# Kernel optimization log

Hardware: AMD Instinct MI355X
Metric: run time of the kernel (lower is better)

Reference implementation:

```python
import jax, jax.numpy as jnp
import numpy as np

N_NODES = 100000
N_EDGES = 1600000
IN_FEATS = 128
H_FEATS = 128


def setup_inputs() -> dict:
    key = jax.random.key(0)
    ks = jax.random.split(key, 8)
    s_in = 1.0 / np.sqrt(IN_FEATS)
    s_h = 1.0 / np.sqrt(H_FEATS)
    return {
        "emb_weight": jax.random.normal(ks[0], (N_NODES, IN_FEATS), jnp.float32),
        "W1_self": jax.random.normal(ks[1], (IN_FEATS, H_FEATS), jnp.float32) * s_in,
        "W1_neigh": jax.random.normal(ks[2], (IN_FEATS, H_FEATS), jnp.float32) * s_in,
        "b1": jnp.zeros((H_FEATS,), jnp.float32),
        "W2_self": jax.random.normal(ks[3], (H_FEATS, H_FEATS), jnp.float32) * s_h,
        "W2_neigh": jax.random.normal(ks[4], (H_FEATS, H_FEATS), jnp.float32) * s_h,
        "b2": jnp.zeros((H_FEATS,), jnp.float32),
        "edges": jax.random.randint(ks[5], (2, N_EDGES), 0, N_NODES, jnp.int64)
            if jax.config.jax_enable_x64 else
            jax.random.randint(ks[5], (2, N_EDGES), 0, N_NODES, jnp.int32),
    }


def _sage_conv(h, src, dst, W_self, W_neigh, b):
    # DGL SAGEConv(mean): out = h @ W_self + mean_neigh(h) @ W_neigh + b
    agg = jax.ops.segment_sum(h[src], dst, num_segments=N_NODES)  # [N, F]
    deg = jax.ops.segment_sum(jnp.ones((src.shape[0],), h.dtype), dst,
                              num_segments=N_NODES)
    mean = agg / jnp.maximum(deg, 1.0)[:, None]  # zero-in-degree -> zeros
    return h @ W_self + mean @ W_neigh + b


def reference(emb_weight, W1_self, W1_neigh, b1, W2_self, W2_neigh, b2, edges):
    src, dst = edges[0], edges[1]
    h = emb_weight  # node_emb(g.nodes()) over all nodes
    h = _sage_conv(h, src, dst, W1_self, W1_neigh, b1)
    h = jax.nn.leaky_relu(h, negative_slope=0.2)
    # dropout is identity in eval mode
    h = _sage_conv(h, src, dst, W2_self, W2_neigh, b2)
    return h
```

## Files before the change

kernel.cpp:

```cpp
#include <hip/hip_runtime.h>
#include <hip/hip_bf16.h>

#define N_NODES_C 100000
#define FEATS 128
#define SH 10
#define NBK 128
#define PB  256
#define CAST_BLOCKS 12500

typedef unsigned int uint32;
typedef __bf16 bf16_t;
typedef bf16_t bf16x8 __attribute__((ext_vector_type(8)));
typedef float f32x4 __attribute__((ext_vector_type(4)));

union Frag { uint4 u; bf16x8 v; };

__device__ __forceinline__ unsigned short f32_to_bf16_bits(float f) {
    uint32 u = __float_as_uint(f);
    u += 0x7fffu + ((u >> 16) & 1u);
    return (unsigned short)(u >> 16);
}
__device__ __forceinline__ float bf16_lo(uint32 p) { return __uint_as_float(p << 16); }
__device__ __forceinline__ float bf16_hi(uint32 p) { return __uint_as_float(p & 0xffff0000u); }

__global__ __launch_bounds__(256) void prep_fused(
    const int* __restrict__ dst, int* __restrict__ gHist, int nE, int chunk,
    const float4* __restrict__ emb4, unsigned short* __restrict__ hb0, int n4,
    const float* __restrict__ W1s, const float* __restrict__ W1n, unsigned short* __restrict__ wt1,
    const float* __restrict__ W2s, const float* __restrict__ W2n, unsigned short* __restrict__ wt2)
{
    __shared__ int h[NBK];
    const int b = blockIdx.x;
    const int tid = threadIdx.x;

    if (b < PB) {
        if (tid < NBK) h[tid] = 0;
        __syncthreads();
        const int b0 = b * chunk;
        const int e1 = min(b0 + chunk, nE);
        for (int e = b0 + tid; e < e1; e += 256)
            atomicAdd(&h[dst[e] >> SH], 1);
        __syncthreads();
        if (tid < NBK) gHist[tid * PB + b] = h[tid];
    } else if (b < PB + 32) {
        const int which = (b - PB) >> 4;
        const float* Ws = which ? W2s : W1s;
        const float* Wn = which ? W2n : W1n;
        unsigned short* wt = which ? wt2 : wt1;
        int gid = ((b - PB) & 15) * 256 + tid;
        int frag = gid >> 6, lane = gid & 63;
        int nt = frag >> 3, ks = frag & 7;
        int n = nt * 16 + (lane & 15);
        int kbase = ks * 32 + (lane >> 4) * 8;
        union { unsigned short s[8]; uint4 u; } o;
#pragma unroll
        for (int j = 0; j < 8; ++j) {
            int k = kbase + j;
            float v = (k < 128) ? Ws[(size_t)k * FEATS + n] : Wn[(size_t)(k - 128) * FEATS + n];
            o.s[j] = f32_to_bf16_bits(v);
        }
        *(uint4*)(wt + (size_t)gid * 8) = o.u;
    } else {
        int i = (b - PB - 32) * 256 + tid;
        if (i >= n4) return;
        float4 v = emb4[i];
        union { unsigned short s[4]; uint2 u; } o;
        o.s[0] = f32_to_bf16_bits(v.x);
        o.s[1] = f32_to_bf16_bits(v.y);
        o.s[2] = f32_to_bf16_bits(v.z);
        o.s[3] = f32_to_bf16_bits(v.w);
        *(uint2*)(hb0 + (size_t)i * 4) = o.u;
    }
}

__global__ __launch_bounds__(1024) void scan_one(int* __restrict__ g) {
    __shared__ int ss[1024];
    const int tid = threadIdx.x;
    const int base = tid * 32;
    int pref[32];
    int sum = 0;
#pragma unroll
    for (int j = 0; j < 32; ++j) {
        int v = g[base + j];
        pref[j] = sum;
        sum += v;
    }
    ss[tid] = sum;
    __syncthreads();
    for (int d = 1; d < 1024; d <<= 1) {
        int t = (tid >= d) ? ss[tid - d] : 0;
        __syncthreads();
        ss[tid] += t;
        __syncthreads();
    }
    int ex = ss[tid] - sum;
#pragma unroll
    for (int j = 0; j < 32; ++j)
        g[base + j] = ex + pref[j];
}

__global__ __launch_bounds__(1024) void part_scatter(const int* __restrict__ src,
                                                     const int* __restrict__ dst,
                                                     const int* __restrict__ gScan,
                                                     uint32* __restrict__ ebuf,
                                                     int nE, int chunk) {
    __shared__ int cur[NBK];
    const int tid = threadIdx.x;
    if (tid < NBK) cur[tid] = gScan[tid * PB + blockIdx.x];
    __syncthreads();
    const int b0 = blockIdx.x * chunk;
    const int e1 = min(b0 + chunk, nE);
    for (int e = b0 + tid; e < e1; e += 1024) {
        int d = dst[e];
        int pos = atomicAdd(&cur[d >> SH], 1);
        ebuf[pos] = (uint32)src[e] | ((uint32)(d & ((1 << SH) - 1)) << 17);
    }
}

__global__ __launch_bounds__(1024) void bucket_csr(const uint32* __restrict__ ebuf,
                                                   const int* __restrict__ gScan,
                                                   int* __restrict__ off,
                                                   int* __restrict__ csr,
                                                   int nE) {
    __shared__ int cnt[1 << SH];
    __shared__ int ss[1 << SH];
    const int b = blockIdx.x;
    const int tid = threadIdx.x;
    const int start = gScan[b * PB];
    const int end = gScan[(b + 1) * PB];
    const int nodeBase = b << SH;
    cnt[tid] = 0;
    __syncthreads();
    for (int e = start + tid; e < end; e += 1024)
        atomicAdd(&cnt[ebuf[e] >> 17], 1);
    __syncthreads();
    int own = cnt[tid];
    ss[tid] = own;
    __syncthreads();
    for (int d = 1; d < 1024; d <<= 1) {
        int t = (tid >= d) ? ss[tid - d] : 0;
        __syncthreads();
        ss[tid] += t;
        __syncthreads();
    }
    int ex = ss[tid] - own;
    cnt[tid] = ex;
    int node = nodeBase + tid;
    if (node < N_NODES_C) off[node] = start + ex;
    if (b == gridDim.x - 1 && tid == 0) off[N_NODES_C] = nE;
    __syncthreads();
    for (int e = start + tid; e < end; e += 1024) {
        uint32 p = ebuf[e];
        int pos = atomicAdd(&cnt[p >> 17], 1);
        csr[start + pos] = (int)((p & 0x1FFFFu) << 8);
    }
}

__global__ __launch_bounds__(256) void gather_mean_w2(const unsigned short* __restrict__ hb,
                                                      const int* __restrict__ csrB,
                                                      const int* __restrict__ off,
                                                      unsigned short* __restrict__ meanb,
                                                      int nNodes) {
    const int node = blockIdx.x * 4 + (threadIdx.x >> 6);
    const int lane = threadIdx.x & 63;
    if (node >= nNodes) return;
    const int start = __builtin_amdgcn_readfirstlane(off[node]);
    const int end   = __builtin_amdgcn_readfirstlane(off[node + 1]);
    const int half = lane >> 5;
    const int c = lane & 31;
    const char* base = (const char*)hb + (size_t)(c * 8);
    float a0 = 0.f, a1 = 0.f, a2 = 0.f, a3 = 0.f;
    int e = start;
    for (; e + 16 <= end; e += 16) {
        const int o0  = csrB[e + 0],  o1  = csrB[e + 1],  o2  = csrB[e + 2],  o3  = csrB[e + 3];
        const int o4  = csrB[e + 4],  o5  = csrB[e + 5],  o6  = csrB[e + 6],  o7  = csrB[e + 7];
        const int o8  = csrB[e + 8],  o9  = csrB[e + 9],  o10 = csrB[e + 10], o11 = csrB[e + 11];
        const int o12 = csrB[e + 12], o13 = csrB[e + 13], o14 = csrB[e + 14], o15 = csrB[e + 15];
        const uint2 u0 = *(const uint2*)(base + (size_t)(half ? o1  : o0));
        const uint2 u1 = *(const uint2*)(base + (size_t)(half ? o3  : o2));
        const uint2 u2 = *(const uint2*)(base + (size_t)(half ? o5  : o4));
        const uint2 u3 = *(const uint2*)(base + (size_t)(half ? o7  : o6));
        const uint2 u4 = *(const uint2*)(base + (size_t)(half ? o9  : o8));
        const uint2 u5 = *(const uint2*)(base + (size_t)(half ? o11 : o10));
        const uint2 u6 = *(const uint2*)(base + (size_t)(half ? o13 : o12));
        const uint2 u7 = *(const uint2*)(base + (size_t)(half ? o15 : o14));
        a0 += bf16_lo(u0.x); a1 += bf16_hi(u0.x); a2 += bf16_lo(u0.y); a3 += bf16_hi(u0.y);
        a0 += bf16_lo(u1.x); a1 += bf16_hi(u1.x); a2 += bf16_lo(u1.y); a3 += bf16_hi(u1.y);
        a0 += bf16_lo(u2.x); a1 += bf16_hi(u2.x); a2 += bf16_lo(u2.y); a3 += bf16_hi(u2.y);
        a0 += bf16_lo(u3.x); a1 += bf16_hi(u3.x); a2 += bf16_lo(u3.y); a3 += bf16_hi(u3.y);
        a0 += bf16_lo(u4.x); a1 += bf16_hi(u4.x); a2 += bf16_lo(u4.y); a3 += bf16_hi(u4.y);
        a0 += bf16_lo(u5.x); a1 += bf16_hi(u5.x); a2 += bf16_lo(u5.y); a3 += bf16_hi(u5.y);
        a0 += bf16_lo(u6.x); a1 += bf16_hi(u6.x); a2 += bf16_lo(u6.y); a3 += bf16_hi(u6.y);
        a0 += bf16_lo(u7.x); a1 += bf16_hi(u7.x); a2 += bf16_lo(u7.y); a3 += bf16_hi(u7.y);
    }
    if (e + 8 <= end) {
        const int o0 = csrB[e + 0], o1 = csrB[e + 1], o2 = csrB[e + 2], o3 = csrB[e + 3];
        const int o4 = csrB[e + 4], o5 = csrB[e + 5], o6 = csrB[e + 6], o7 = csrB[e + 7];
        const uint2 u0 = *(const uint2*)(base + (size_t)(half ? o1 : o0));
        const uint2 u1 = *(const uint2*)(base + (size_t)(half ? o3 : o2));
        const uint2 u2 = *(const uint2*)(base + (size_t)(half ? o5 : o4));
        const uint2 u3 = *(const uint2*)(base + (size_t)(half ? o7 : o6));
        a0 += bf16_lo(u0.x); a1 += bf16_hi(u0.x); a2 += bf16_lo(u0.y); a3 += bf16_hi(u0.y);
        a0 += bf16_lo(u1.x); a1 += bf16_hi(u1.x); a2 += bf16_lo(u1.y); a3 += bf16_hi(u1.y);
        a0 += bf16_lo(u2.x); a1 += bf16_hi(u2.x); a2 += bf16_lo(u2.y); a3 += bf16_hi(u2.y);
        a0 += bf16_lo(u3.x); a1 += bf16_hi(u3.x); a2 += bf16_lo(u3.y); a3 += bf16_hi(u3.y);
        e += 8;
    }
    if (e + 4 <= end) {
        const int o0 = csrB[e + 0], o1 = csrB[e + 1], o2 = csrB[e + 2], o3 = csrB[e + 3];
        const uint2 u0 = *(const uint2*)(base + (size_t)(half ? o1 : o0));
        const uint2 u1 = *(const uint2*)(base + (size_t)(half ? o3 : o2));
        a0 += bf16_lo(u0.x); a1 += bf16_hi(u0.x); a2 += bf16_lo(u0.y); a3 += bf16_hi(u0.y);
        a0 += bf16_lo(u1.x); a1 += bf16_hi(u1.x); a2 += bf16_lo(u1.y); a3 += bf16_hi(u1.y);
        e += 4;
    }
    if (e + 2 <= end) {
        const int o0 = csrB[e + 0], o1 = csrB[e + 1];
        const uint2 u = *(const uint2*)(base + (size_t)(half ? o1 : o0));
        a0 += bf16_lo(u.x); a1 += bf16_hi(u.x); a2 += bf16_lo(u.y); a3 += bf16_hi(u.y);
        e += 2;
    }
    if (e < end && half == 0) {
        const uint2 u = *(const uint2*)(base + (size_t)csrB[e]);
        a0 += bf16_lo(u.x); a1 += bf16_hi(u.x); a2 += bf16_lo(u.y); a3 += bf16_hi(u.y);
    }
    a0 += __shfl_xor(a0, 32);
    a1 += __shfl_xor(a1, 32);
    a2 += __shfl_xor(a2, 32);
    a3 += __shfl_xor(a3, 32);
    const int deg = end - start;
    const float invd = (deg > 0) ? (1.f / (float)deg) : 0.f;
    if (half == 0) {
        uint2 o;
        o.x = ((uint32)f32_to_bf16_bits(a1 * invd) << 16) | (uint32)f32_to_bf16_bits(a0 * invd);
        o.y = ((uint32)f32_to_bf16_bits(a3 * invd) << 16) | (uint32)f32_to_bf16_bits(a2 * invd);
        ((uint2*)meanb)[(size_t)node * 32 + c] = o;
    }
}

__global__ __launch_bounds__(512) void sage_gemm_mfma(const unsigned short* __restrict__ HB,
                                                      const unsigned short* __restrict__ MB,
                                                      const unsigned short* __restrict__ WT,
                                                      const float* __restrict__ bias,
                                                      void* __restrict__ OUTP,
                                                      int nNodes, int mode) {
    __shared__ uint4 wtl[4096];
    const int tid = threadIdx.x;
    const uint4* wt4 = (const uint4*)WT;
#pragma unroll
    for (int i = 0; i < 8; ++i)
        wtl[i * 512 + tid] = wt4[i * 512 + tid];

    const int wave = tid >> 6;
    const int lane = tid & 63;
    const int waveBase = blockIdx.x * 128 + wave * 16;
    const int m = lane & 15;
    const int quad = lane >> 4;

    int arow = waveBase + m;
    if (arow >= nNodes) arow = nNodes - 1;
    const uint4* hrow = (const uint4*)(HB + (size_t)arow * FEATS);
    const uint4* mrow = (const uint4*)(MB + (size_t)arow * FEATS);

    Frag a[8];
#pragma unroll
    for (int ks = 0; ks < 4; ++ks) a[ks].u = hrow[ks * 4 + quad];
#pragma unroll
    for (int ks = 0; ks < 4; ++ks) a[ks + 4].u = mrow[ks * 4 + quad];

    __syncthreads();

    f32x4 acc[8];
#pragma unroll
    for (int nt = 0; nt < 8; ++nt) acc[nt] = (f32x4){0.f, 0.f, 0.f, 0.f};

#pragma unroll
    for (int ks = 0; ks < 8; ++ks) {
#pragma unroll
        for (int nt = 0; nt < 8; ++nt) {
            Frag b;
            b.u = wtl[(nt * 8 + ks) * 64 + lane];
            acc[nt] = __builtin_amdgcn_mfma_f32_16x16x32_bf16(a[ks].v, b.v, acc[nt], 0, 0, 0);
        }
    }

#pragma unroll
    for (int nt = 0; nt < 8; ++nt) {
        const int col = nt * 16 + m;
        const float bv = bias[col];
#pragma unroll
        for (int r = 0; r < 4; ++r) {
            const int grow = waveBase + quad * 4 + r;
            if (grow >= nNodes) continue;
            float v = acc[nt][r] + bv;
            if (mode) {
                v = v > 0.f ? v : 0.2f * v;
                ((unsigned short*)OUTP)[(size_t)grow * FEATS + col] = f32_to_bf16_bits(v);
            } else {
                ((float*)OUTP)[(size_t)grow * FEATS + col] = v;
            }
        }
    }
}

extern "C" void kernel_launch(void* const* d_in, const int* in_sizes, int n_in,
                              void* d_out, int out_size, void* d_ws, size_t ws_size,
                              hipStream_t stream) {
    const float* emb = (const float*)d_in[0];
    const float* W1s = (const float*)d_in[1];
    const float* W1n = (const float*)d_in[2];
    const float* b1  = (const float*)d_in[3];
    const float* W2s = (const float*)d_in[4];
    const float* W2n = (const float*)d_in[5];
    const float* b2  = (const float*)d_in[6];
    const int*   edg = (const int*)d_in[7];

    const int nE = in_sizes[7] / 2;
    const int* src = edg;
    const int* dst = edg + nE;

    const int chunk = (nE + PB - 1) / PB;
    const int nActB = (N_NODES_C + (1 << SH) - 1) >> SH;
    const int n4 = N_NODES_C * FEATS / 4;

    const size_t bfTab = (size_t)N_NODES_C * FEATS * sizeof(unsigned short);

    char* ws = (char*)d_ws;
    int* off      = (int*)(ws);
    int* gHist    = (int*)(ws + (512 << 10));
    int* csr      = (int*)(ws + (1 << 20));
    uint32* ebuf  = (uint32*)(ws + (8 << 20));
    unsigned short* wt1 = (unsigned short*)(ws + (15 << 20));
    unsigned short* wt2 = (unsigned short*)(ws + (15 << 20) + (64 << 10));
    unsigned short* hb0 = (unsigned short*)(ws + (16 << 20));
    unsigned short* h1b = (unsigned short*)((char*)hb0 + bfTab);
    unsigned short* mnb = (unsigned short*)((char*)h1b + bfTab);
    float* out = (float*)d_out;

    prep_fused<<<PB + 32 + CAST_BLOCKS, 256, 0, stream>>>(
        dst, gHist, nE, chunk, (const float4*)emb, hb0, n4,
        W1s, W1n, wt1, W2s, W2n, wt2);

    scan_one<<<1, 1024, 0, stream>>>(gHist);
    part_scatter<<<PB, 1024, 0, stream>>>(src, dst, gHist, ebuf, nE, chunk);
    bucket_csr<<<nActB, 1024, 0, stream>>>(ebuf, gHist, off, csr, nE);

    const int gatherBlocks = (N_NODES_C + 3) / 4;
    const int gemmBlocks = (N_NODES_C + 127) / 128;

    gather_mean_w2<<<gatherBlocks, 256, 0, stream>>>(hb0, csr, off, mnb, N_NODES_C);
    sage_gemm_mfma<<<gemmBlocks, 512, 0, stream>>>(hb0, mnb, wt1, b1, h1b, N_NODES_C, 1);

    gather_mean_w2<<<gatherBlocks, 256, 0, stream>>>(h1b, csr, off, mnb, N_NODES_C);
    sage_gemm_mfma<<<gemmBlocks, 512, 0, stream>>>(h1b, mnb, wt2, b2, out, N_NODES_C, 0);
}
```

Before: 321.4 us.

## Fold global scan into scatter blocks and make GEMM persistent over row stripes

Removes the single-block scan kernel: every part_scatter block now redundantly scans the 32K-entry histogram and keeps only its own bucket cursors, and block 0 writes the bucket start offsets for bucket_csr. The GEMM becomes a grid-stride persistent kernel with 512 blocks, so each block loads the weight tile into LDS once and reuses it across several 128-row stripes. This saves a launch and a serial single-block step, and cuts the number of weight tile loads. In exchange each scatter block repeats the scan, and the GEMM no longer overlaps one stripe's A loads with another block's work as naturally.

```diff
diff --git a/kernel.cpp b/kernel.cpp
--- a/kernel.cpp
+++ b/kernel.cpp
@@ -73,40 +73,48 @@
     }
 }
 
-__global__ __launch_bounds__(1024) void scan_one(int* __restrict__ g) {
+__global__ __launch_bounds__(1024) void part_scatter(const int* __restrict__ src,
+                                                     const int* __restrict__ dst,
+                                                     const int* __restrict__ gHist,
+                                                     int* __restrict__ bstart,
+                                                     uint32* __restrict__ ebuf,
+                                                     int nE, int chunk) {
     __shared__ int ss[1024];
+    __shared__ int cur[NBK];
     const int tid = threadIdx.x;
     const int base = tid * 32;
     int pref[32];
-    int sum = 0;
-#pragma unroll
-    for (int j = 0; j < 32; ++j) {
-        int v = g[base + j];
-        pref[j] = sum;
-        sum += v;
-    }
-    ss[tid] = sum;
-    __syncthreads();
-    for (int d = 1; d < 1024; d <<= 1) {
-        int t = (tid >= d) ? ss[tid - d] : 0;
-        __syncthreads();
-        ss[tid] += t;
-        __syncthreads();
-    }
-    int ex = ss[tid] - sum;
-#pragma unroll
-    for (int j = 0; j < 32; ++j)
-        g[base + j] = ex + pref[j];
-}
-
-__global__ __launch_bounds__(1024) void part_scatter(const int* __restrict__ src,
-                                                     const int* __restrict__ dst,
-                                                     const int* __restrict__ gScan,
-                                                     uint32* __restrict__ ebuf,
-                                                     int nE, int chunk) {
-    __shared__ int cur[NBK];
-    const int tid = threadIdx.x;
-    if (tid < NBK) cur[tid] = gScan[tid * PB + blockIdx.x];
+    {
+        int sum = 0;
+#pragma unroll
+        for (int j = 0; j < 32; ++j) {
+            int v = gHist[base + j];
+            pref[j] = sum;
+            sum += v;
+        }
+        ss[tid] = sum;
+        __syncthreads();
+        for (int d = 1; d < 1024; d <<= 1) {
+            int t = (tid >= d) ? ss[tid - d] : 0;
+            __syncthreads();
+            ss[tid] += t;
+            __syncthreads();
+        }
+        const int ex = ss[tid] - sum;
+#pragma unroll
+        for (int j = 0; j < 32; ++j) {
+            const int f = base + j;
+            const int v = ex + pref[j];
+            if ((f & (PB - 1)) == blockIdx.x) cur[f >> 8] = v;
+        }
+        if (blockIdx.x == 0) {
+#pragma unroll
+            for (int j = 0; j < 32; ++j) {
+                const int f = base + j;
+                if ((f & (PB - 1)) == 0) bstart[f >> 8] = ex + pref[j];
+            }
+        }
+    }
     __syncthreads();
     const int b0 = blockIdx.x * chunk;
     const int e1 = min(b0 + chunk, nE);
@@ -118,7 +126,7 @@
 }
 
 __global__ __launch_bounds__(1024) void bucket_csr(const uint32* __restrict__ ebuf,
-                                                   const int* __restrict__ gScan,
+                                                   const int* __restrict__ bstart,
                                                    int* __restrict__ off,
                                                    int* __restrict__ csr,
                                                    int nE) {
@@ -126,8 +134,8 @@
     __shared__ int ss[1 << SH];
     const int b = blockIdx.x;
     const int tid = threadIdx.x;
-    const int start = gScan[b * PB];
-    const int end = gScan[(b + 1) * PB];
+    const int start = bstart[b];
+    const int end = bstart[b + 1];
     const int nodeBase = b << SH;
     cnt[tid] = 0;
     __syncthreads();
@@ -243,7 +251,7 @@
                                                       const unsigned short* __restrict__ WT,
                                                       const float* __restrict__ bias,
                                                       void* __restrict__ OUTP,
-                                                      int nNodes, int mode) {
+                                                      int nNodes, int nStripes, int mode) {
     __shared__ uint4 wtl[4096];
     const int tid = threadIdx.x;
     const uint4* wt4 = (const uint4*)WT;
@@ -253,51 +261,54 @@
 
     const int wave = tid >> 6;
     const int lane = tid & 63;
-    const int waveBase = blockIdx.x * 128 + wave * 16;
     const int m = lane & 15;
     const int quad = lane >> 4;
 
-    int arow = waveBase + m;
-    if (arow >= nNodes) arow = nNodes - 1;
-    const uint4* hrow = (const uint4*)(HB + (size_t)arow * FEATS);
-    const uint4* mrow = (const uint4*)(MB + (size_t)arow * FEATS);
-
-    Frag a[8];
-#pragma unroll
-    for (int ks = 0; ks < 4; ++ks) a[ks].u = hrow[ks * 4 + quad];
-#pragma unroll
-    for (int ks = 0; ks < 4; ++ks) a[ks + 4].u = mrow[ks * 4 + quad];
-
-    __syncthreads();
-
-    f32x4 acc[8];
-#pragma unroll
-    for (int nt = 0; nt < 8; ++nt) acc[nt] = (f32x4){0.f, 0.f, 0.f, 0.f};
-
-#pragma unroll
-    for (int ks = 0; ks < 8; ++ks) {
+    __syncthreads();
+
+    for (int stripe = blockIdx.x; stripe < nStripes; stripe += gridDim.x) {
+        const int waveBase = stripe * 128 + wave * 16;
+
+        int arow = waveBase + m;
+        if (arow >= nNodes) arow = nNodes - 1;
+        const uint4* hrow = (const uint4*)(HB + (size_t)arow * FEATS);
+        const uint4* mrow = (const uint4*)(MB + (size_t)arow * FEATS);
+
+        Frag a[8];
+#pragma unroll
+        for (int ks = 0; ks < 4; ++ks) a[ks].u = hrow[ks * 4 + quad];
+#pragma unroll
+        for (int ks = 0; ks < 4; ++ks) a[ks + 4].u = mrow[ks * 4 + quad];
+
+        f32x4 acc[8];
+#pragma unroll
+        for (int nt = 0; nt < 8; ++nt) acc[nt] = (f32x4){0.f, 0.f, 0.f, 0.f};
+
+#pragma unroll
+        for (int ks = 0; ks < 8; ++ks) {
+#pragma unroll
+            for (int nt = 0; nt < 8; ++nt) {
+                Frag b;
+                b.u = wtl[(nt * 8 + ks) * 64 + lane];
+                acc[nt] = __builtin_amdgcn_mfma_f32_16x16x32_bf16(a[ks].v, b.v, acc[nt], 0, 0, 0);
+            }
+        }
+
 #pragma unroll
         for (int nt = 0; nt < 8; ++nt) {
-            Frag b;
-            b.u = wtl[(nt * 8 + ks) * 64 + lane];
-            acc[nt] = __builtin_amdgcn_mfma_f32_16x16x32_bf16(a[ks].v, b.v, acc[nt], 0, 0, 0);
-        }
-    }
-
-#pragma unroll
-    for (int nt = 0; nt < 8; ++nt) {
-        const int col = nt * 16 + m;
-        const float bv = bias[col];
-#pragma unroll
-        for (int r = 0; r < 4; ++r) {
-            const int grow = waveBase + quad * 4 + r;
-            if (grow >= nNodes) continue;
-            float v = acc[nt][r] + bv;
-            if (mode) {
-                v = v > 0.f ? v : 0.2f * v;
-                ((unsigned short*)OUTP)[(size_t)grow * FEATS + col] = f32_to_bf16_bits(v);
-            } else {
-                ((float*)OUTP)[(size_t)grow * FEATS + col] = v;
+            const int col = nt * 16 + m;
+            const float bv = bias[col];
+#pragma unroll
+            for (int r = 0; r < 4; ++r) {
+                const int grow = waveBase + quad * 4 + r;
+                if (grow >= nNodes) continue;
+                float v = acc[nt][r] + bv;
+                if (mode) {
+                    v = v > 0.f ? v : 0.2f * v;
+                    ((unsigned short*)OUTP)[(size_t)grow * FEATS + col] = f32_to_bf16_bits(v);
+                } else {
+                    ((float*)OUTP)[(size_t)grow * FEATS + col] = v;
+                }
             }
         }
     }
@@ -328,6 +339,7 @@
     char* ws = (char*)d_ws;
     int* off      = (int*)(ws);
     int* gHist    = (int*)(ws + (512 << 10));
+    int* bstart   = (int*)(ws + (768 << 10));
     int* csr      = (int*)(ws + (1 << 20));
     uint32* ebuf  = (uint32*)(ws + (8 << 20));
     unsigned short* wt1 = (unsigned short*)(ws + (15 << 20));
@@ -341,16 +353,16 @@
         dst, gHist, nE, chunk, (const float4*)emb, hb0, n4,
         W1s, W1n, wt1, W2s, W2n, wt2);
 
-    scan_one<<<1, 1024, 0, stream>>>(gHist);
-    part_scatter<<<PB, 1024, 0, stream>>>(src, dst, gHist, ebuf, nE, chunk);
-    bucket_csr<<<nActB, 1024, 0, stream>>>(ebuf, gHist, off, csr, nE);
+    part_scatter<<<PB, 1024, 0, stream>>>(src, dst, gHist, bstart, ebuf, nE, chunk);
+    bucket_csr<<<nActB, 1024, 0, stream>>>(ebuf, bstart, off, csr, nE);
 
     const int gatherBlocks = (N_NODES_C + 3) / 4;
-    const int gemmBlocks = (N_NODES_C + 127) / 128;
+    const int nStripes = (N_NODES_C + 127) / 128;
+    const int gemmBlocks = 512;
 
     gather_mean_w2<<<gatherBlocks, 256, 0, stream>>>(hb0, csr, off, mnb, N_NODES_C);
-    sage_gemm_mfma<<<gemmBlocks, 512, 0, stream>>>(hb0, mnb, wt1, b1, h1b, N_NODES_C, 1);
+    sage_gemm_mfma<<<gemmBlocks, 512, 0, stream>>>(hb0, mnb, wt1, b1, h1b, N_NODES_C, nStripes, 1);
 
     gather_mean_w2<<<gatherBlocks, 256, 0, stream>>>(h1b, csr, off, mnb, N_NODES_C);
-    sage_gemm_mfma<<<gemmBlocks, 512, 0, stream>>>(h1b, mnb, wt2, b2, out, N_NODES_C, 0);
-}
+    sage_gemm_mfma<<<gemmBlocks, 512, 0, stream>>>(h1b, mnb, wt2, b2, out, N_NODES_C, nStripes, 0);
+}
```

New measurement: 381.3 us. 18.6% more time.
